# Performance work log

Hardware: AMD Instinct MI355X
Metric: run time of the kernel (lower is better)

Reference implementation:

```python
import jax, jax.numpy as jnp
import numpy as np

LOG2 = float(np.log(2.0))
INV_SQRT3 = float(1.0 / np.sqrt(3.0))

def ssp(x):
    # ShiftedSoftPlus: softplus(x) - log(2)
    return jax.nn.softplus(x) - LOG2

def setup_inputs() -> dict:
    key = jax.random.key(0)
    ks = jax.random.split(key, 13)
    N, E, M, A, R, H = 50000, 800000, 32, 16, 8, 64
    return {
        "node_feats": jax.random.normal(ks[0], (N, 4 * M), dtype=jnp.float32),  # 32x0e + 32x1o flat
        "node_attrs": jax.random.normal(ks[1], (N, A), dtype=jnp.float32),
        "edge_embedding": jax.random.uniform(ks[2], (E, R), dtype=jnp.float32),  # radial basis, 0e
        "edge_attrs": jax.random.normal(ks[3], (E, 4), dtype=jnp.float32),  # SH: 1x0e + 1x1o
        "edge_index": jax.random.randint(ks[4], (2, E), 0, N),
        "W1s": jax.random.normal(ks[5], (M, M), dtype=jnp.float32),
        "W1v": jax.random.normal(ks[6], (M, M), dtype=jnp.float32),
        "Wr0": jax.random.normal(ks[7], (R, H), dtype=jnp.float32),
        "Wr1": jax.random.normal(ks[8], (H, 4 * M), dtype=jnp.float32),  # tp.weight_numel = 4 paths * 32 mul
        "W2s": jax.random.normal(ks[9], (2 * M, M), dtype=jnp.float32),
        "W2v": jax.random.normal(ks[10], (2 * M, M), dtype=jnp.float32),
        "Wsc_s": jax.random.normal(ks[11], (M, A, M), dtype=jnp.float32),
        "Wsc_v": jax.random.normal(ks[12], (M, A, M), dtype=jnp.float32),
    }

def reference(node_feats, node_attrs, edge_embedding, edge_attrs, edge_index,
              W1s, W1v, Wr0, Wr1, W2s, W2v, Wsc_s, Wsc_v):
    N = node_feats.shape[0]
    M = 32           # multiplicity of each irrep
    A = node_attrs.shape[1]
    AVG_NEIGH = 16.0
    # split flat irreps features: [N,32] scalars (0e), [N,32,3] vectors (1o)
    s_in = node_feats[:, :M]
    v_in = node_feats[:, M:].reshape(N, M, 3)

    # linear_1: per-irrep channel mixing, e3nn 1/sqrt(fan_in) normalization
    inv_m = 1.0 / float(np.sqrt(M))
    s = (s_in @ W1s) * inv_m                                  # [N,32]
    v = jnp.einsum('nmc,mk->nkc', v_in, W1v) * inv_m          # [N,32,3]

    # radial MLP on edge scalars -> per-edge tensor-product path weights [E,4,32]
    h = ssp((edge_embedding @ Wr0) * (1.0 / float(np.sqrt(edge_embedding.shape[1]))))
    w = (h @ Wr1) * (1.0 / float(np.sqrt(h.shape[1])))
    w = w.reshape(-1, 4, M)
    w0, w1, w2, w3 = w[:, 0], w[:, 1], w[:, 2], w[:, 3]

    src, dst = edge_index[0], edge_index[1]
    ss = s[src]                                               # [E,32]
    vv = v[src]                                               # [E,32,3]
    e0 = edge_attrs[:, :1]                                    # [E,1]  Y_0
    e1 = edge_attrs[:, 1:4]                                   # [E,3]  Y_1

    # weighted CG tensor product, 'uvu' paths (component normalization)
    m0 = w0 * ss * e0                                                   # 0e x 0e -> 0e
    m3 = w3 * jnp.einsum('emc,ec->em', vv, e1) * INV_SQRT3              # 1o x 1o -> 0e
    m1 = w1[:, :, None] * ss[:, :, None] * e1[:, None, :]               # 0e x 1o -> 1o
    m2 = w2[:, :, None] * vv * e0[:, :, None]                           # 1o x 0e -> 1o
    mid_s = jnp.concatenate([m0, m3], axis=1)                           # [E,64]
    mid_v = jnp.concatenate([m1, m2], axis=1)                           # [E,64,3]

    # scatter-sum to destination nodes
    ns = jax.ops.segment_sum(mid_s, dst, num_segments=N)
    nv = jax.ops.segment_sum(mid_v, dst, num_segments=N)
    neigh = 1.0 / float(np.sqrt(AVG_NEIGH))

    # linear_2 on simplified mid irreps 64x0e + 64x1o
    inv2 = 1.0 / float(np.sqrt(2 * M))
    out_s = (ns @ W2s) * (inv2 * neigh)
    out_v = jnp.einsum('nmc,mk->nkc', nv, W2v) * (inv2 * neigh)

    # self connection: FullyConnectedTensorProduct(node_feats_in, node_attrs)
    fc = 1.0 / float(np.sqrt(M * A))
    out_s = out_s + jnp.einsum('nu,na,uaw->nw', s_in, node_attrs, Wsc_s) * fc
    out_v = out_v + jnp.einsum('nuc,na,uaw->nwc', v_in, node_attrs, Wsc_v) * fc

    return jnp.concatenate([out_s, out_v.reshape(N, 3 * M)], axis=1)
```

## Files before the change

### kernel.cpp

```cpp
#include <hip/hip_runtime.h>
#include <stdint.h>
#include <math.h>

typedef __attribute__((ext_vector_type(8))) short bf16x8;
typedef __attribute__((ext_vector_type(4))) float f32x4;

__device__ __forceinline__ unsigned short f2bf(float f){
  unsigned int u = __float_as_uint(f);
  u += 0x7fffu + ((u >> 16) & 1u);
  return (unsigned short)(u >> 16);
}

__device__ __forceinline__ float bf2f(short s){
  return __uint_as_float(((unsigned int)(unsigned short)s) << 16);
}

__device__ __forceinline__ float ssp_f(float x){
  float u = exp2f(-fabsf(x)*1.4426950408889634f);
  return fmaxf(x, 0.f) + 0.6931471805599453f*(__log2f(1.0f + u) - 1.0f);
}

__global__ void k_count(const int* __restrict__ eidx, int E, int* __restrict__ cnt){
  int e = blockIdx.x*256 + threadIdx.x;
  if(e < E) atomicAdd(&cnt[eidx[E + e]], 1);
}

__global__ void k_scan_a(const int* __restrict__ cnt, int N, int* __restrict__ offs, int* __restrict__ bsum){
  __shared__ int arr[1024];
  int t = threadIdx.x, i = blockIdx.x*1024 + t;
  int v = (i < N) ? cnt[i] : 0;
  int own = v;
  arr[t] = v;
  for(int off = 1; off < 1024; off <<= 1){
    __syncthreads();
    int u = (t >= off) ? arr[t - off] : 0;
    __syncthreads();
    arr[t] += u;
  }
  if(i < N) offs[i] = arr[t] - own;
  if(t == 1023) bsum[blockIdx.x] = arr[1023];
}

__global__ void k_scan_b(int* __restrict__ bsum, int NB, int* __restrict__ offs, int N){
  if(threadIdx.x == 0 && blockIdx.x == 0){
    int run = 0;
    for(int b = 0; b < NB; b++){ int t = bsum[b]; bsum[b] = run; run += t; }
    offs[N] = run;
  }
}

__global__ void k_scan_c(int* __restrict__ offs, const int* __restrict__ bsum, int* __restrict__ cursor, int N){
  int i = blockIdx.x*1024 + threadIdx.x;
  if(i < N){
    int v = offs[i] + bsum[blockIdx.x];
    offs[i] = v;
    cursor[i] = v;
  }
}

__global__ void k_perm(const float* __restrict__ eemb, const float* __restrict__ eattr,
                       const int* __restrict__ eidx, int E, int* __restrict__ cursor,
                       int* __restrict__ src_perm, float* __restrict__ eattr_perm,
                       float* __restrict__ eemb_perm){
  int e = blockIdx.x*256 + threadIdx.x;
  if(e < E){
    int d = eidx[E + e];
    int dp = atomicAdd(&cursor[d], 1);
    src_perm[dp] = eidx[e];
    *(f32x4*)(eattr_perm + (size_t)dp*4) = *(const f32x4*)(eattr + (size_t)e*4);
    *(f32x4*)(eemb_perm + (size_t)dp*8)     = *(const f32x4*)(eemb + (size_t)e*8);
    *(f32x4*)(eemb_perm + (size_t)dp*8 + 4) = *(const f32x4*)(eemb + (size_t)e*8 + 4);
  }
}

__global__ void k_prepw(const float* __restrict__ Wr0, const float* __restrict__ Wr1,
                        const float* __restrict__ Wsc_s, const float* __restrict__ Wsc_v,
                        unsigned short* __restrict__ wr1frag, float* __restrict__ wr0p,
                        unsigned short* __restrict__ wscfrag){
  int id = blockIdx.x*256 + threadIdx.x;
  if(id < 512) wr0p[id] = Wr0[(id & 7)*64 + (id >> 3)];
  if(id < 1024){
    int fi = id >> 6, lane = id & 63;
    int c0 = lane & 15, g = lane >> 4;
    int kt = fi >> 3, ct = fi & 7;
    unsigned short tmp[8];
    #pragma unroll
    for(int i = 0; i < 8; i++){
      int k = kt*32 + g*8 + i;
      tmp[i] = f2bf(Wr1[k*128 + ct*16 + c0]);
    }
    #pragma unroll
    for(int i = 0; i < 8; i++) wr1frag[id*8 + i] = tmp[i];
  }
  {
    int sel  = id >> 11;
    int fi   = (id >> 6) & 31;
    int lane = id & 63;
    int c0 = lane & 15, g = lane >> 4;
    int ks = fi >> 1, ct = fi & 1;
    const float* W = sel ? Wsc_v : Wsc_s;
    bf16x8 tmp;
    #pragma unroll
    for(int i = 0; i < 8; i++){
      int k = ks*32 + g*8 + i;
      tmp[i] = (short)f2bf(W[k*32 + ct*16 + c0]);
    }
    *(bf16x8*)&wscfrag[(size_t)id*8] = tmp;
  }
}

__global__ __launch_bounds__(256) void k_node(
    const float* __restrict__ nf, const float* __restrict__ na,
    const float* __restrict__ W1s, const float* __restrict__ W1v,
    const unsigned short* __restrict__ wscfrag,
    unsigned short* __restrict__ sv, float* __restrict__ out, int N)
{
  __shared__ float xl[64*133];
  __shared__ __align__(16) float al[64*20];
  const int t = threadIdx.x;
  const int n0 = blockIdx.x*64;

  for(int idx = t; idx < 64*128; idx += 256){
    int r = idx >> 7, c = idx & 127;
    int n = n0 + r;
    xl[r*133 + c] = (n < N) ? nf[(size_t)n*128 + c] : 0.f;
  }
  for(int idx = t; idx < 64*16; idx += 256){
    int r = idx >> 4, c = idx & 15;
    int n = n0 + r;
    al[r*20 + c] = (n < N) ? na[(size_t)n*16 + c] : 0.f;
  }
  __syncthreads();

  const float INVM = 0.17677669529663689f;
  const float FC   = 0.044194173824159216f;

  {
    int node = t & 63;
    int wvq  = t >> 6;
    if(n0 + node < N){
      unsigned short* svr = sv + (size_t)(n0+node)*128;
      for(int j = 0; j < 8; j++){
        int q  = wvq + 4*j;
        int k0 = q*4;
        float a0=0.f, a1=0.f, a2=0.f, a3=0.f;
        if(k0 < 32){
          for(int m = 0; m < 32; m++){
            float xv = xl[node*133 + m];
            f32x4 w4 = *(const f32x4*)&W1s[m*32 + k0];
            a0 += xv*w4[0]; a1 += xv*w4[1]; a2 += xv*w4[2]; a3 += xv*w4[3];
          }
        } else {
          int cc = (k0-32) >> 5, kk = (k0-32) & 31;
          for(int m = 0; m < 32; m++){
            float xv = xl[node*133 + 32 + 3*m + cc];
            f32x4 w4 = *(const f32x4*)&W1v[m*32 + kk];
            a0 += xv*w4[0]; a1 += xv*w4[1]; a2 += xv*w4[2]; a3 += xv*w4[3];
          }
        }
        int q16 = k0 >> 4;
        int cb  = k0 & 15;
        svr[(cb+0)*8 + q16] = f2bf(a0*INVM);
        svr[(cb+1)*8 + q16] = f2bf(a1*INVM);
        svr[(cb+2)*8 + q16] = f2bf(a2*INVM);
        svr[(cb+3)*8 + q16] = f2bf(a3*INVM);
      }
    }
  }

  const int lane = t & 63, wv = t >> 6;
  const int c0 = lane & 15, g = lane >> 4;
  const unsigned short* wf = wscfrag + (size_t)((wv == 0) ? 0 : 16384);

  f32x4 accm[4][2];
  #pragma unroll
  for(int rt = 0; rt < 4; rt++)
    #pragma unroll
    for(int ct = 0; ct < 2; ct++) accm[rt][ct] = (f32x4){0.f,0.f,0.f,0.f};

  for(int ks = 0; ks < 16; ks++){
    bf16x8 bfr[2];
    bfr[0] = *(const bf16x8*)&wf[(size_t)((ks*2 + 0)*64 + lane)*8];
    bfr[1] = *(const bf16x8*)&wf[(size_t)((ks*2 + 1)*64 + lane)*8];
    int u2 = ks*2 + (g >> 1);
    int ab = (g & 1)*8;
    #pragma unroll
    for(int rt = 0; rt < 4; rt++){
      int row = rt*16 + c0;
      float xv = (wv == 0) ? xl[row*133 + u2] : xl[row*133 + 32 + 3*u2 + (wv-1)];
      f32x4 v0 = *(const f32x4*)&al[row*20 + ab];
      f32x4 v1 = *(const f32x4*)&al[row*20 + ab + 4];
      bf16x8 a;
      a[0] = (short)f2bf(xv*v0[0]); a[1] = (short)f2bf(xv*v0[1]);
      a[2] = (short)f2bf(xv*v0[2]); a[3] = (short)f2bf(xv*v0[3]);
      a[4] = (short)f2bf(xv*v1[0]); a[5] = (short)f2bf(xv*v1[1]);
      a[6] = (short)f2bf(xv*v1[2]); a[7] = (short)f2bf(xv*v1[3]);
      #pragma unroll
      for(int ct = 0; ct < 2; ct++)
        accm[rt][ct] = __builtin_amdgcn_mfma_f32_16x16x32_bf16(a, bfr[ct], accm[rt][ct], 0, 0, 0);
    }
  }

  #pragma unroll
  for(int rt = 0; rt < 4; rt++)
    #pragma unroll
    for(int ct = 0; ct < 2; ct++)
      #pragma unroll
      for(int i = 0; i < 4; i++){
        int node = n0 + rt*16 + g*4 + i;
        if(node < N){
          int col = ct*16 + c0;
          float v = accm[rt][ct][i] * FC;
          if(wv == 0) out[(size_t)node*128 + col] = v;
          else        out[(size_t)node*128 + 32 + 3*col + (wv-1)] = v;
        }
      }
}

__global__ __launch_bounds__(256, 4) void k_wedge(
    const float* __restrict__ eemb_perm,
    const unsigned short* __restrict__ wr1frag, const float* __restrict__ wr0p,
    unsigned short* __restrict__ wper, int NB16, int E)
{
  __shared__ __align__(16) float wr0t[512];
  __shared__ __align__(16) unsigned short bwl[8192];
  const int t = threadIdx.x;
  {
    const f32x4* s4 = (const f32x4*)wr1frag;
    f32x4* d4 = (f32x4*)bwl;
    #pragma unroll
    for(int i = 0; i < 4; i++) d4[t + i*256] = s4[t + i*256];
    if(t < 128) ((f32x4*)wr0t)[t] = ((const f32x4*)wr0p)[t];
  }
  __syncthreads();

  const int lane = t & 63;
  const int wv   = t >> 6;
  const int c0   = lane & 15;
  const int g    = lane >> 4;
  const float S8 = 0.35355339059327373f;

  int p = blockIdx.x*4 + wv;
  if(p >= NB16) return;
  int p16 = p*16;
  int bc = E - p16; if(bc > 16) bc = 16;
  bool val = (c0 < bc);

  size_t row = (size_t)(p16 + (val ? c0 : 0))*8;
  f32x4 p0 = *(const f32x4*)(eemb_perm + row);
  f32x4 p1 = *(const f32x4*)(eemb_perm + row + 4);
  float ee[8];
  ee[0]=p0[0]; ee[1]=p0[1]; ee[2]=p0[2]; ee[3]=p0[3];
  ee[4]=p1[0]; ee[5]=p1[1]; ee[6]=p1[2]; ee[7]=p1[3];

  bf16x8 afr[2];
  #pragma unroll
  for(int kt = 0; kt < 2; kt++){
    bf16x8 a;
    #pragma unroll
    for(int i = 0; i < 8; i++){
      int j = kt*32 + g*8 + i;
      f32x4 wa = *(const f32x4*)&wr0t[j*8];
      f32x4 wb = *(const f32x4*)&wr0t[j*8 + 4];
      float pre = ee[0]*wa[0] + ee[1]*wa[1] + ee[2]*wa[2] + ee[3]*wa[3]
                + ee[4]*wb[0] + ee[5]*wb[1] + ee[6]*wb[2] + ee[7]*wb[3];
      a[i] = (short)f2bf(ssp_f(pre * S8));
    }
    afr[kt] = a;
  }

  f32x4 cfr[8];
  #pragma unroll
  for(int ct = 0; ct < 8; ct++) cfr[ct] = (f32x4){0.f,0.f,0.f,0.f};
  #pragma unroll
  for(int kt = 0; kt < 2; kt++)
    #pragma unroll
    for(int ct = 0; ct < 8; ct++){
      bf16x8 bfr = *(const bf16x8*)&bwl[((kt*8 + ct)*64 + lane)*8];
      cfr[ct] = __builtin_amdgcn_mfma_f32_16x16x32_bf16(afr[kt], bfr, cfr[ct], 0, 0, 0);
    }

  #pragma unroll
  for(int i = 0; i < 4; i++){
    if(g*4 + i < bc){
      bf16x8 wpk;
      #pragma unroll
      for(int ct = 0; ct < 8; ct++) wpk[ct] = (short)f2bf(cfr[ct][i] * 0.125f);
      *(bf16x8*)(wper + (size_t)(p16 + g*4 + i)*128 + c0*8) = wpk;
    }
  }
}

__global__ __launch_bounds__(256, 4) void k_msg(
    const unsigned short* __restrict__ sv, const unsigned short* __restrict__ wper,
    const float* __restrict__ eattr_perm, const int* __restrict__ src_perm,
    const int* __restrict__ offs, const float* __restrict__ W2s,
    const float* __restrict__ W2v, float* __restrict__ out, int N)
{
  __shared__ __align__(16) float nsl[4][256];
  __shared__ __align__(16) float w2sT[32*68];
  __shared__ __align__(16) float w2vT[32*68];
  const int t = threadIdx.x, lane = t & 63, wv = t >> 6;
  const int c0 = lane & 15, g = lane >> 4;

  {
    #pragma unroll
    for(int i = 0; i < 8; i++){
      int idx = t + i*256;
      int m = idx >> 5, o = idx & 31;
      w2sT[o*68 + m] = W2s[idx];
      w2vT[o*68 + m] = W2v[idx];
    }
  }
  __syncthreads();

  const int n = blockIdx.x*4 + wv;
  if(n >= N) return;

  const float SC2 = 0.03125f;
  const float IS3 = 0.57735026918962576f;

  float acc[16];
  #pragma unroll
  for(int i = 0; i < 16; i++) acc[i] = 0.f;

  const int eb0 = offs[n], eb1 = offs[n+1];
  for(int eb = eb0; eb < eb1; eb += 16){
    int bc = eb1 - eb; if(bc > 16) bc = 16;
    #pragma unroll
    for(int r = 0; r < 4; r++){
      int es = r*4 + g;
      if(es >= bc) continue;
      int e = eb + es;
      int s = src_perm[e];
      bf16x8 sr = *(const bf16x8*)(sv + (size_t)s*128 + c0*8);
      f32x4 ea = *(const f32x4*)(eattr_perm + (size_t)e*4);
      bf16x8 w8 = *(const bf16x8*)(wper + (size_t)e*128 + c0*8);
      float w0A = bf2f(w8[0]), w0B = bf2f(w8[1]);
      float w1A = bf2f(w8[2]), w1B = bf2f(w8[3]);
      float w2A = bf2f(w8[4]), w2B = bf2f(w8[5]);
      float w3A = bf2f(w8[6]), w3B = bf2f(w8[7]);
      float ssA = bf2f(sr[0]), ssB = bf2f(sr[1]);
      float vA0 = bf2f(sr[2]), vB0 = bf2f(sr[3]);
      float vA1 = bf2f(sr[4]), vB1 = bf2f(sr[5]);
      float vA2 = bf2f(sr[6]), vB2 = bf2f(sr[7]);
      float e0 = ea[0], e1x = ea[1], e1y = ea[2], e1z = ea[3];

      acc[0] += w0A*ssA*e0;
      acc[1] += w0B*ssB*e0;
      acc[2] += w3A*(vA0*e1x + vA1*e1y + vA2*e1z);
      acc[3] += w3B*(vB0*e1x + vB1*e1y + vB2*e1z);
      float h1A = w1A*ssA, h1B = w1B*ssB;
      acc[4]  += h1A*e1x; acc[5]  += h1A*e1y; acc[6]  += h1A*e1z;
      acc[7]  += h1B*e1x; acc[8]  += h1B*e1y; acc[9]  += h1B*e1z;
      float h2A = w2A*e0, h2B = w2B*e0;
      acc[10] += h2A*vA0; acc[11] += h2A*vA1; acc[12] += h2A*vA2;
      acc[13] += h2B*vB0; acc[14] += h2B*vB1; acc[15] += h2B*vB2;
    }
  }

  #pragma unroll
  for(int i = 0; i < 16; i++){
    acc[i] += __shfl_xor(acc[i], 16);
    acc[i] += __shfl_xor(acc[i], 32);
  }

  float* nl = nsl[wv];
  if(g == 0){
    nl[c0]      = acc[0];
    nl[16 + c0] = acc[1];
    nl[32 + c0] = acc[2]*IS3;
    nl[48 + c0] = acc[3]*IS3;
    #pragma unroll
    for(int cc = 0; cc < 3; cc++){
      nl[64 + cc*64 +  0 + c0] = acc[4  + cc];
      nl[64 + cc*64 + 16 + c0] = acc[7  + cc];
      nl[64 + cc*64 + 32 + c0] = acc[10 + cc];
      nl[64 + cc*64 + 48 + c0] = acc[13 + cc];
    }
  }
  __threadfence_block();

  const int t1 = lane, t2 = 64 + lane;
  int u1 = t1 - 32; if(u1 < 0) u1 = 0;
  const int w1i = u1/3, c1i = u1%3;
  const int w2i = (t2 - 32)/3, c2i = (t2 - 32)%3;
  const f32x4* p1a = (const f32x4*)((t1 < 32) ? &nl[0] : &nl[64 + c1i*64]);
  const f32x4* p1b = (const f32x4*)((t1 < 32) ? &w2sT[t1*68] : &w2vT[w1i*68]);
  const f32x4* p2a = (const f32x4*)&nl[64 + c2i*64];
  const f32x4* p2b = (const f32x4*)&w2vT[w2i*68];
  float s1 = 0.f, s2 = 0.f;
  #pragma unroll
  for(int q = 0; q < 16; q++){
    f32x4 a = p1a[q], b = p1b[q];
    f32x4 c = p2a[q], d = p2b[q];
    s1 += a[0]*b[0] + a[1]*b[1] + a[2]*b[2] + a[3]*b[3];
    s2 += c[0]*d[0] + c[1]*d[1] + c[2]*d[2] + c[3]*d[3];
  }
  out[(size_t)n*128 + t1] += s1*SC2;
  out[(size_t)n*128 + t2] += s2*SC2;
}

extern "C" void kernel_launch(void* const* d_in, const int* in_sizes, int n_in,
                              void* d_out, int out_size, void* d_ws, size_t ws_size,
                              hipStream_t stream)
{
  const float* nf    = (const float*)d_in[0];
  const float* na    = (const float*)d_in[1];
  const float* eemb  = (const float*)d_in[2];
  const float* eattr = (const float*)d_in[3];
  const int*   eidx  = (const int*)d_in[4];
  const float* W1s   = (const float*)d_in[5];
  const float* W1v   = (const float*)d_in[6];
  const float* Wr0   = (const float*)d_in[7];
  const float* Wr1   = (const float*)d_in[8];
  const float* W2s   = (const float*)d_in[9];
  const float* W2v   = (const float*)d_in[10];
  const float* Wsc_s = (const float*)d_in[11];
  const float* Wsc_v = (const float*)d_in[12];
  float* out = (float*)d_out;

  int N = in_sizes[0]/128;
  int E = in_sizes[2]/8;
  int NB16 = (E + 15)/16;

  char* ws = (char*)d_ws;
  size_t off = 0;
  unsigned short* sv = (unsigned short*)(ws + off); off += (size_t)N*128*2;
  unsigned short* wper = (unsigned short*)(ws + off); off += (size_t)NB16*16*128*2;
  float* eemb_perm = (float*)(ws + off);      off += (size_t)NB16*16*8*4;
  float* eattr_perm = (float*)(ws + off);     off += (size_t)NB16*16*4*4;
  int* src_perm = (int*)(ws + off);           off += (size_t)NB16*16*4;
  int* cnt    = (int*)(ws + off);             off += (size_t)N*4;
  int* offs   = (int*)(ws + off);             off += (size_t)(N+1)*4;
  int* cursor = (int*)(ws + off);             off += (size_t)N*4;
  int* bsum   = (int*)(ws + off);             off += 4096;
  unsigned short* wr1frag = (unsigned short*)(ws + off); off += 16384;
  float* wr0p = (float*)(ws + off);           off += 2048;
  unsigned short* wscfrag = (unsigned short*)(ws + off); off += 65536;

  int NB = (N + 1023)/1024;

  k_prepw  <<<dim3(16),          dim3(256), 0, stream>>>(Wr0, Wr1, Wsc_s, Wsc_v,
                                                         wr1frag, wr0p, wscfrag);
  (void)hipMemsetAsync(cnt, 0, (size_t)N*4, stream);
  k_count  <<<dim3((E+255)/256), dim3(256), 0, stream>>>(eidx, E, cnt);
  k_scan_a <<<dim3(NB),          dim3(1024),0, stream>>>(cnt, N, offs, bsum);
  k_scan_b <<<dim3(1),           dim3(64),  0, stream>>>(bsum, NB, offs, N);
  k_scan_c <<<dim3(NB),          dim3(1024),0, stream>>>(offs, bsum, cursor, N);
  k_perm   <<<dim3((E+255)/256), dim3(256), 0, stream>>>(eemb, eattr, eidx, E, cursor,
                                                         src_perm, eattr_perm, eemb_perm);
  k_node   <<<dim3((N+63)/64),   dim3(256), 0, stream>>>(nf, na, W1s, W1v, wscfrag, sv, out, N);
  k_wedge  <<<dim3((NB16+3)/4),  dim3(256), 0, stream>>>(eemb_perm, wr1frag, wr0p, wper, NB16, E);
  k_msg    <<<dim3((N+3)/4),     dim3(256), 0, stream>>>(sv, wper, eattr_perm, src_perm, offs,
                                                         W2s, W2v, out, N);
}
```

Measured before the change: 365.7 us.

## Use MFMA for linear_1 in node kernel and fuse weight prep into count

The per-node linear_1 (scalar and vector channel mixing) moves from scalar FP32 FMA loops to bf16 MFMA 16x16x32 using pre-packed weight fragments. The weight-prep kernel is merged into the edge-count kernel, which saves one launch. Node features are rounded to bf16 before the matmul, so this adds precision loss on the sv path, which was already stored as bf16.

New measurement: 337.9 us. -7.6%, faster.

```diff
diff --git a/kernel.cpp b/kernel.cpp
--- a/kernel.cpp
+++ b/kernel.cpp
@@ -20,9 +20,55 @@
   return fmaxf(x, 0.f) + 0.6931471805599453f*(__log2f(1.0f + u) - 1.0f);
 }
 
-__global__ void k_count(const int* __restrict__ eidx, int E, int* __restrict__ cnt){
-  int e = blockIdx.x*256 + threadIdx.x;
-  if(e < E) atomicAdd(&cnt[eidx[E + e]], 1);
+__global__ void k_count_prep(const int* __restrict__ eidx, int E, int* __restrict__ cnt,
+                             const float* __restrict__ Wr0, const float* __restrict__ Wr1,
+                             const float* __restrict__ Wsc_s, const float* __restrict__ Wsc_v,
+                             const float* __restrict__ W1s, const float* __restrict__ W1v,
+                             unsigned short* __restrict__ wr1frag, float* __restrict__ wr0p,
+                             unsigned short* __restrict__ wscfrag, unsigned short* __restrict__ w1frag){
+  int id = blockIdx.x*256 + threadIdx.x;
+  if(id < 512) wr0p[id] = Wr0[(id & 7)*64 + (id >> 3)];
+  if(id < 1024){
+    int fi = id >> 6, lane = id & 63;
+    int c0 = lane & 15, g = lane >> 4;
+    int kt = fi >> 3, ct = fi & 7;
+    unsigned short tmp[8];
+    #pragma unroll
+    for(int i = 0; i < 8; i++){
+      int k = kt*32 + g*8 + i;
+      tmp[i] = f2bf(Wr1[k*128 + ct*16 + c0]);
+    }
+    #pragma unroll
+    for(int i = 0; i < 8; i++) wr1frag[id*8 + i] = tmp[i];
+  }
+  if(id < 4096){
+    int sel  = id >> 11;
+    int fi   = (id >> 6) & 31;
+    int lane = id & 63;
+    int c0 = lane & 15, g = lane >> 4;
+    int ks = fi >> 1, ct = fi & 1;
+    const float* W = sel ? Wsc_v : Wsc_s;
+    bf16x8 tmp;
+    #pragma unroll
+    for(int i = 0; i < 8; i++){
+      int k = ks*32 + g*8 + i;
+      tmp[i] = (short)f2bf(W[k*32 + ct*16 + c0]);
+    }
+    *(bf16x8*)&wscfrag[(size_t)id*8] = tmp;
+  }
+  if(id < 256){
+    int sel = id >> 7, ct = (id >> 6) & 1, lane = id & 63;
+    int c0 = lane & 15, g = lane >> 4;
+    const float* W = sel ? W1v : W1s;
+    bf16x8 tmp;
+    #pragma unroll
+    for(int i = 0; i < 8; i++){
+      int m = g*8 + i;
+      tmp[i] = (short)f2bf(W[m*32 + ct*16 + c0]);
+    }
+    *(bf16x8*)&w1frag[(size_t)id*8] = tmp;
+  }
+  if(id < E) atomicAdd(&cnt[eidx[E + id]], 1);
 }
 
 __global__ void k_scan_a(const int* __restrict__ cnt, int N, int* __restrict__ offs, int* __restrict__ bsum){
@@ -73,45 +119,9 @@
   }
 }
 
-__global__ void k_prepw(const float* __restrict__ Wr0, const float* __restrict__ Wr1,
-                        const float* __restrict__ Wsc_s, const float* __restrict__ Wsc_v,
-                        unsigned short* __restrict__ wr1frag, float* __restrict__ wr0p,
-                        unsigned short* __restrict__ wscfrag){
-  int id = blockIdx.x*256 + threadIdx.x;
-  if(id < 512) wr0p[id] = Wr0[(id & 7)*64 + (id >> 3)];
-  if(id < 1024){
-    int fi = id >> 6, lane = id & 63;
-    int c0 = lane & 15, g = lane >> 4;
-    int kt = fi >> 3, ct = fi & 7;
-    unsigned short tmp[8];
-    #pragma unroll
-    for(int i = 0; i < 8; i++){
-      int k = kt*32 + g*8 + i;
-      tmp[i] = f2bf(Wr1[k*128 + ct*16 + c0]);
-    }
-    #pragma unroll
-    for(int i = 0; i < 8; i++) wr1frag[id*8 + i] = tmp[i];
-  }
-  {
-    int sel  = id >> 11;
-    int fi   = (id >> 6) & 31;
-    int lane = id & 63;
-    int c0 = lane & 15, g = lane >> 4;
-    int ks = fi >> 1, ct = fi & 1;
-    const float* W = sel ? Wsc_v : Wsc_s;
-    bf16x8 tmp;
-    #pragma unroll
-    for(int i = 0; i < 8; i++){
-      int k = ks*32 + g*8 + i;
-      tmp[i] = (short)f2bf(W[k*32 + ct*16 + c0]);
-    }
-    *(bf16x8*)&wscfrag[(size_t)id*8] = tmp;
-  }
-}
-
 __global__ __launch_bounds__(256) void k_node(
     const float* __restrict__ nf, const float* __restrict__ na,
-    const float* __restrict__ W1s, const float* __restrict__ W1v,
+    const unsigned short* __restrict__ w1frag,
     const unsigned short* __restrict__ wscfrag,
     unsigned short* __restrict__ sv, float* __restrict__ out, int N)
 {
@@ -135,41 +145,37 @@
   const float INVM = 0.17677669529663689f;
   const float FC   = 0.044194173824159216f;
 
-  {
-    int node = t & 63;
-    int wvq  = t >> 6;
-    if(n0 + node < N){
-      unsigned short* svr = sv + (size_t)(n0+node)*128;
-      for(int j = 0; j < 8; j++){
-        int q  = wvq + 4*j;
-        int k0 = q*4;
-        float a0=0.f, a1=0.f, a2=0.f, a3=0.f;
-        if(k0 < 32){
-          for(int m = 0; m < 32; m++){
-            float xv = xl[node*133 + m];
-            f32x4 w4 = *(const f32x4*)&W1s[m*32 + k0];
-            a0 += xv*w4[0]; a1 += xv*w4[1]; a2 += xv*w4[2]; a3 += xv*w4[3];
-          }
-        } else {
-          int cc = (k0-32) >> 5, kk = (k0-32) & 31;
-          for(int m = 0; m < 32; m++){
-            float xv = xl[node*133 + 32 + 3*m + cc];
-            f32x4 w4 = *(const f32x4*)&W1v[m*32 + kk];
-            a0 += xv*w4[0]; a1 += xv*w4[1]; a2 += xv*w4[2]; a3 += xv*w4[3];
-          }
-        }
-        int q16 = k0 >> 4;
-        int cb  = k0 & 15;
-        svr[(cb+0)*8 + q16] = f2bf(a0*INVM);
-        svr[(cb+1)*8 + q16] = f2bf(a1*INVM);
-        svr[(cb+2)*8 + q16] = f2bf(a2*INVM);
-        svr[(cb+3)*8 + q16] = f2bf(a3*INVM);
-      }
-    }
-  }
-
   const int lane = t & 63, wv = t >> 6;
   const int c0 = lane & 15, g = lane >> 4;
+
+  {
+    const unsigned short* w1f = w1frag + (size_t)((wv == 0) ? 0 : 1024);
+    bf16x8 b0 = *(const bf16x8*)&w1f[(0*64 + lane)*8];
+    bf16x8 b1 = *(const bf16x8*)&w1f[(1*64 + lane)*8];
+    #pragma unroll
+    for(int rt = 0; rt < 4; rt++){
+      int row = rt*16 + c0;
+      bf16x8 a;
+      #pragma unroll
+      for(int i = 0; i < 8; i++){
+        int m = g*8 + i;
+        float xv = (wv == 0) ? xl[row*133 + m] : xl[row*133 + 32 + 3*m + (wv-1)];
+        a[i] = (short)f2bf(xv);
+      }
+      f32x4 z = {0.f,0.f,0.f,0.f};
+      f32x4 d0 = __builtin_amdgcn_mfma_f32_16x16x32_bf16(a, b0, z, 0, 0, 0);
+      f32x4 d1 = __builtin_amdgcn_mfma_f32_16x16x32_bf16(a, b1, z, 0, 0, 0);
+      #pragma unroll
+      for(int r = 0; r < 4; r++){
+        int node = n0 + rt*16 + g*4 + r;
+        if(node < N){
+          sv[(size_t)node*128 + c0*8 + wv*2 + 0] = f2bf(d0[r]*INVM);
+          sv[(size_t)node*128 + c0*8 + wv*2 + 1] = f2bf(d1[r]*INVM);
+        }
+      }
+    }
+  }
+
   const unsigned short* wf = wscfrag + (size_t)((wv == 0) ? 0 : 16384);
 
   f32x4 accm[4][2];
@@ -438,19 +444,20 @@
   unsigned short* wr1frag = (unsigned short*)(ws + off); off += 16384;
   float* wr0p = (float*)(ws + off);           off += 2048;
   unsigned short* wscfrag = (unsigned short*)(ws + off); off += 65536;
+  unsigned short* w1frag = (unsigned short*)(ws + off);  off += 4096;
 
   int NB = (N + 1023)/1024;
 
-  k_prepw  <<<dim3(16),          dim3(256), 0, stream>>>(Wr0, Wr1, Wsc_s, Wsc_v,
-                                                         wr1frag, wr0p, wscfrag);
   (void)hipMemsetAsync(cnt, 0, (size_t)N*4, stream);
-  k_count  <<<dim3((E+255)/256), dim3(256), 0, stream>>>(eidx, E, cnt);
+  k_count_prep<<<dim3((E+255)/256), dim3(256), 0, stream>>>(eidx, E, cnt, Wr0, Wr1,
+                                                            Wsc_s, Wsc_v, W1s, W1v,
+                                                            wr1frag, wr0p, wscfrag, w1frag);
   k_scan_a <<<dim3(NB),          dim3(1024),0, stream>>>(cnt, N, offs, bsum);
   k_scan_b <<<dim3(1),           dim3(64),  0, stream>>>(bsum, NB, offs, N);
   k_scan_c <<<dim3(NB),          dim3(1024),0, stream>>>(offs, bsum, cursor, N);
   k_perm   <<<dim3((E+255)/256), dim3(256), 0, stream>>>(eemb, eattr, eidx, E, cursor,
                                                          src_perm, eattr_perm, eemb_perm);
-  k_node   <<<dim3((N+63)/64),   dim3(256), 0, stream>>>(nf, na, W1s, W1v, wscfrag, sv, out, N);
+  k_node   <<<dim3((N+63)/64),   dim3(256), 0, stream>>>(nf, na, w1frag, wscfrag, sv, out, N);
   k_wedge  <<<dim3((NB16+3)/4),  dim3(256), 0, stream>>>(eemb_perm, wr1frag, wr0p, wper, NB16, E);
   k_msg    <<<dim3((N+3)/4),     dim3(256), 0, stream>>>(sv, wper, eattr_perm, src_perm, offs,
                                                          W2s, W2v, out, N);
```
